# Kernel tuning notes

Hardware: AMD Instinct MI355X
Metric: run time of the kernel (lower is better)

## Reference

```python
import jax, jax.numpy as jnp
import numpy as np

B, H, W, D, C = 1, 32, 32, 32, 256
WS = (8, 8, 8)
SS = (4, 4, 4)
NH = 8
HD = C // NH
N = WS[0] * WS[1] * WS[2]
NW = (H // WS[0]) * (W // WS[1]) * (D // WS[2])


def _rel_pos_index():
    coords = np.stack(np.meshgrid(np.arange(WS[0]), np.arange(WS[1]), np.arange(WS[2]), indexing='ij'))
    cf = coords.reshape(3, -1)
    rc = (cf[:, :, None] - cf[:, None, :]).transpose(1, 2, 0).astype(np.int64)
    rc[:, :, 0] += WS[0] - 1
    rc[:, :, 1] += WS[1] - 1
    rc[:, :, 2] += WS[2] - 1
    rc[:, :, 0] *= (2 * WS[2] - 1) * (2 * WS[1] - 1)
    rc[:, :, 1] *= (2 * WS[2] - 1)
    return rc.sum(-1).reshape(-1)  # [N*N]


def _attn_mask():
    m = np.zeros((H, W, D), np.float32)
    cnt = 0

    def sl(ws, ss):
        return ((0, -ws), (-ws, -ss), (-ss, None))

    for hs in sl(WS[0], SS[0]):
        for ws_ in sl(WS[1], SS[1]):
            for ds in sl(WS[2], SS[2]):
                m[hs[0]:hs[1], ws_[0]:ws_[1], ds[0]:ds[1]] = cnt
                cnt += 1
    m = m.reshape(H // WS[0], WS[0], W // WS[1], WS[1], D // WS[2], WS[2])
    m = m.transpose(0, 2, 4, 1, 3, 5).reshape(NW, N)
    diff = m[:, None, :] - m[:, :, None]  # [NW, N, N]
    return np.where(diff != 0, -100.0, 0.0).astype(np.float32)


REL_IDX = jnp.asarray(_rel_pos_index())
ATTN_MASK = jnp.asarray(_attn_mask())  # [NW, N, N]


def setup_inputs() -> dict:
    key = jax.random.key(0)
    ks = jax.random.split(key, 4)
    return {
        'x': jax.random.normal(ks[0], (B, H, W, D, C), jnp.float32),
        'qkv_weight': jax.random.normal(ks[1], (3 * C, C), jnp.float32) * 0.02,
        'qkv_bias': jnp.zeros((3 * C,), jnp.float32),
        'proj_weight': jax.random.normal(ks[2], (C, C), jnp.float32) * 0.02,
        'proj_bias': jnp.zeros((C,), jnp.float32),
        'rpb_table': jax.random.normal(ks[3], ((2 * WS[0] - 1) * (2 * WS[1] - 1) * (2 * WS[2] - 1), NH), jnp.float32) * 0.02,
    }


def reference(x, qkv_weight, qkv_bias, proj_weight, proj_bias, rpb_table):
    # cyclic shift
    xs = jnp.roll(x, (-SS[0], -SS[1], -SS[2]), axis=(1, 2, 3))
    # window partition -> [B*NW, N, C]
    xw = xs.reshape(B, H // WS[0], WS[0], W // WS[1], WS[1], D // WS[2], WS[2], C)
    xw = xw.transpose(0, 1, 3, 5, 2, 4, 6, 7).reshape(B * NW, N, C)
    # qkv projection
    qkv = xw @ qkv_weight.T + qkv_bias
    qkv = qkv.reshape(B * NW, N, 3, NH, HD).transpose(2, 0, 3, 1, 4)  # [3, B*NW, NH, N, HD]
    q, k, v = qkv[0] * (HD ** -0.5), qkv[1], qkv[2]
    # relative position bias [NH, N, N]
    bias = rpb_table[REL_IDX].reshape(N, N, NH).transpose(2, 0, 1)
    attn = jnp.einsum('whnd,whmd->whnm', q, k) + bias[None]
    # shift mask per window
    attn = attn.reshape(B, NW, NH, N, N) + ATTN_MASK[None, :, None]
    attn = jax.nn.softmax(attn.reshape(B * NW, NH, N, N), axis=-1)
    out = jnp.einsum('whnm,whmd->whnd', attn, v)
    out = out.transpose(0, 2, 1, 3).reshape(B * NW, N, C)
    out = out @ proj_weight.T + proj_bias
    # un-window -> [B, H, W, D, C]
    out = out.reshape(B, H // WS[0], W // WS[1], D // WS[2], WS[0], WS[1], WS[2], C)
    out = out.transpose(0, 1, 4, 2, 5, 3, 6, 7).reshape(B, H, W, D, C)
    # reverse cyclic shift
    return jnp.roll(out, (SS[0], SS[1], SS[2]), axis=(1, 2, 3))
```

## Files before the change

### kernel.cpp

```cpp
#include <hip/hip_runtime.h>

typedef __attribute__((ext_vector_type(8))) short short8;
typedef __attribute__((ext_vector_type(4))) short s4v;
typedef __attribute__((ext_vector_type(2))) uint uint2v;
typedef __attribute__((ext_vector_type(4))) float floatx4;

#define CCH   256
#define QSCALE 0.17677669529663687f
#define LOG2E  1.4426950408889634f

__device__ __forceinline__ unsigned short f2bf(float f) {
    unsigned u = __float_as_uint(f);
    u = u + 0x7fffu + ((u >> 16) & 1u);
    return (unsigned short)(u >> 16);
}

__device__ __forceinline__ uint pk2bf(float a, float b) {
    uint ua = __float_as_uint(a) + 0x8000u;
    uint ub = __float_as_uint(b) + 0x8000u;
    return __builtin_amdgcn_perm(ub, ua, 0x07060302u);
}

__device__ __forceinline__ void gl_lds16(const void* g, void* l) {
    __builtin_amdgcn_global_load_lds((const __attribute__((address_space(1))) void*)g,
                                     (__attribute__((address_space(3))) void*)l, 16, 0, 0);
}

__device__ __forceinline__ int spatial_off(int token) {
    int w = token >> 9, n = token & 511;
    int wh = w >> 4, ww = (w >> 2) & 3, wd = w & 3;
    int h1 = n >> 6, w1 = (n >> 3) & 7, d1 = n & 7;
    int gh = (wh * 8 + h1 + 4) & 31;
    int gw = (ww * 8 + w1 + 4) & 31;
    int gd = (wd * 8 + d1 + 4) & 31;
    return ((gh * 32 + gw) * 32 + gd) * CCH;
}

__global__ __launch_bounds__(256) void xconv(const float* __restrict__ x,
                                             ushort* __restrict__ Xw) {
    int tid = blockIdx.x * 256 + threadIdx.x;
    int token = tid >> 5, c8 = (tid & 31) * 8;
    const float* src = x + spatial_off(token) + c8;
    float4 a = *(const float4*)src;
    float4 b = *(const float4*)(src + 4);
    uint2v lo, hi;
    lo[0] = pk2bf(a.x, a.y);
    lo[1] = pk2bf(a.z, a.w);
    hi[0] = pk2bf(b.x, b.y);
    hi[1] = pk2bf(b.z, b.w);
    uint2v* dst = (uint2v*)(Xw + (size_t)token * 256 + c8);
    dst[0] = lo;
    dst[1] = hi;
}

__global__ __launch_bounds__(256) void wconv(const float* __restrict__ Wq,
                                             const float* __restrict__ Wp,
                                             ushort* __restrict__ Wqb,
                                             ushort* __restrict__ Wpb) {
    int tid = blockIdx.x * 256 + threadIdx.x;
    if (tid < 196608) {
        float s = (tid < 65536) ? (QSCALE * LOG2E) : 1.0f;
        Wqb[tid] = f2bf(Wq[tid] * s);
    } else {
        int i = tid - 196608;
        Wpb[i] = f2bf(Wp[i]);
    }
}

__global__ __launch_bounds__(256) void pair_prep(const float* __restrict__ rpb,
                                                 uint* __restrict__ Up) {
    int tid = blockIdx.x * 256 + threadIdx.x;
    if (tid >= 27000) return;
    int head = tid / 3375, idx = tid - head * 3375;
    uint lo = f2bf(rpb[idx * 8 + head] * LOG2E);
    uint hi = f2bf(rpb[(idx > 0 ? idx - 1 : 0) * 8 + head] * LOG2E);
    Up[tid] = lo | (hi << 16);
}

__global__ __launch_bounds__(256) void gemm_qkv(
    const ushort* __restrict__ A,
    const ushort* __restrict__ Bw,
    const float* __restrict__ bq,
    ushort* __restrict__ Q, ushort* __restrict__ K, ushort* __restrict__ Vf) {
    __shared__ short As[128 * 64];
    __shared__ short Bs[128 * 64];
    const int t = threadIdx.x;
    const int wv = t >> 6, lane = t & 63, quad = lane >> 4, col = lane & 15;
    const int m0 = blockIdx.y * 128, n0 = blockIdx.x * 128;
    const int wm = (wv & 1) * 64, wn = (wv >> 1) * 64;

    floatx4 zf = {0.f, 0.f, 0.f, 0.f};
    floatx4 acc[4][4];
#pragma unroll
    for (int i = 0; i < 4; ++i)
#pragma unroll
        for (int j = 0; j < 4; ++j) acc[i][j] = zf;

    for (int kk = 0; kk < 256; kk += 64) {
        __syncthreads();
#pragma unroll
        for (int i = 0; i < 4; ++i) {
            int s = i * 256 + t;
            int row = s >> 3, qs = s & 7;
            int qg = qs ^ (row & 7);
            gl_lds16(A + (size_t)(m0 + row) * 256 + kk + qg * 8,
                     As + (i * 256 + wv * 64) * 8);
        }
#pragma unroll
        for (int i = 0; i < 4; ++i) {
            int s = i * 256 + t;
            int row = s >> 3, qs = s & 7;
            int qg = qs ^ (row & 7);
            gl_lds16(Bw + (size_t)(n0 + row) * 256 + kk + qg * 8,
                     Bs + (i * 256 + wv * 64) * 8);
        }
        __syncthreads();
#pragma unroll
        for (int h = 0; h < 2; ++h) {
            short8 af[4], bf[4];
#pragma unroll
            for (int mi = 0; mi < 4; ++mi) {
                int row = wm + mi * 16 + col;
                af[mi] = *(const short8*)(As + (row * 8 + ((h * 4 + quad) ^ (row & 7))) * 8);
            }
#pragma unroll
            for (int ni = 0; ni < 4; ++ni) {
                int row = wn + ni * 16 + col;
                bf[ni] = *(const short8*)(Bs + (row * 8 + ((h * 4 + quad) ^ (row & 7))) * 8);
            }
#pragma unroll
            for (int mi = 0; mi < 4; ++mi)
#pragma unroll
                for (int ni = 0; ni < 4; ++ni)
                    acc[mi][ni] = __builtin_amdgcn_mfma_f32_16x16x32_bf16(af[mi], bf[ni], acc[mi][ni], 0, 0, 0);
        }
    }

#pragma unroll
    for (int ni = 0; ni < 4; ++ni) {
        int j = n0 + wn + ni * 16 + col;
        int three = j >> 8, head = (j >> 5) & 7, hd = j & 31;
        float bias = bq[j] * ((j < 256) ? (QSCALE * LOG2E) : 1.0f);
        if (three == 2) {
            int h = hd >> 4, colv = hd & 15;
#pragma unroll
            for (int mi = 0; mi < 4; ++mi) {
                int mb = m0 + wm + mi * 16 + quad * 4;
                int w = mb >> 9, n = mb & 511;
                size_t off = ((size_t)((w * 8 + head) * 64 + (n >> 4) * 2 + h) << 8)
                           + ((((n >> 2) & 3) * 16 + colv) << 2);
                uint2v pv;
                pv[0] = pk2bf(acc[mi][ni][0] + bias, acc[mi][ni][1] + bias);
                pv[1] = pk2bf(acc[mi][ni][2] + bias, acc[mi][ni][3] + bias);
                *(uint2v*)(Vf + off) = pv;
            }
        } else if (three == 1) {
#pragma unroll
            for (int mi = 0; mi < 4; ++mi) {
#pragma unroll
                for (int r = 0; r < 4; ++r) {
                    int m = m0 + wm + mi * 16 + quad * 4 + r;
                    int w = m >> 9, n = m & 511;
                    size_t off = ((size_t)(w * 8 + head) << 14) + ((size_t)(n >> 4) << 9)
                               + (((hd >> 3) * 16 + (n & 15)) << 3) + (hd & 7);
                    K[off] = f2bf(acc[mi][ni][r] + bias);
                }
            }
        } else {
#pragma unroll
            for (int mi = 0; mi < 4; ++mi) {
#pragma unroll
                for (int r = 0; r < 4; ++r) {
                    int m = m0 + wm + mi * 16 + quad * 4 + r;
                    int w = m >> 9, n = m & 511;
                    Q[((size_t)(w * 8 + head) * 512 + n) * 32 + hd] = f2bf(acc[mi][ni][r] + bias);
                }
            }
        }
    }
}

__global__ __launch_bounds__(256) void gemm_proj(
    const ushort* __restrict__ A,
    const ushort* __restrict__ Bw,
    const float* __restrict__ bp,
    float* __restrict__ out) {
    __shared__ short As[128 * 64];
    __shared__ short Bs[128 * 64];
    const int t = threadIdx.x;
    const int wv = t >> 6, lane = t & 63, quad = lane >> 4, col = lane & 15;
    const int m0 = blockIdx.y * 128, n0 = blockIdx.x * 128;
    const int wm = (wv & 1) * 64, wn = (wv >> 1) * 64;

    floatx4 zf = {0.f, 0.f, 0.f, 0.f};
    floatx4 acc[4][4];
#pragma unroll
    for (int i = 0; i < 4; ++i)
#pragma unroll
        for (int j = 0; j < 4; ++j) acc[i][j] = zf;

    for (int kk = 0; kk < 256; kk += 64) {
        __syncthreads();
#pragma unroll
        for (int i = 0; i < 4; ++i) {
            int s = i * 256 + t;
            int row = s >> 3, qs = s & 7;
            int qg = qs ^ (row & 7);
            gl_lds16(A + (size_t)(m0 + row) * 256 + kk + qg * 8,
                     As + (i * 256 + wv * 64) * 8);
        }
#pragma unroll
        for (int i = 0; i < 4; ++i) {
            int s = i * 256 + t;
            int row = s >> 3, qs = s & 7;
            int qg = qs ^ (row & 7);
            gl_lds16(Bw + (size_t)(n0 + row) * 256 + kk + qg * 8,
                     Bs + (i * 256 + wv * 64) * 8);
        }
        __syncthreads();
#pragma unroll
        for (int h = 0; h < 2; ++h) {
            short8 af[4], bf[4];
#pragma unroll
            for (int mi = 0; mi < 4; ++mi) {
                int row = wm + mi * 16 + col;
                af[mi] = *(const short8*)(As + (row * 8 + ((h * 4 + quad) ^ (row & 7))) * 8);
            }
#pragma unroll
            for (int ni = 0; ni < 4; ++ni) {
                int row = wn + ni * 16 + col;
                bf[ni] = *(const short8*)(Bs + (row * 8 + ((h * 4 + quad) ^ (row & 7))) * 8);
            }
#pragma unroll
            for (int mi = 0; mi < 4; ++mi)
#pragma unroll
                for (int ni = 0; ni < 4; ++ni)
                    acc[mi][ni] = __builtin_amdgcn_mfma_f32_16x16x32_bf16(af[mi], bf[ni], acc[mi][ni], 0, 0, 0);
        }
    }

#pragma unroll
    for (int ni = 0; ni < 4; ++ni) {
        int j = n0 + wn + ni * 16 + col;
        float bias = bp[j];
#pragma unroll
        for (int mi = 0; mi < 4; ++mi) {
#pragma unroll
            for (int r = 0; r < 4; ++r) {
                int m = m0 + wm + mi * 16 + quad * 4 + r;
                out[spatial_off(m) + j] = acc[mi][ni][r] + bias;
            }
        }
    }
}

__global__ __launch_bounds__(512, 2) void attn_kernel(
    const ushort* __restrict__ Q, const ushort* __restrict__ K,
    const ushort* __restrict__ Vf, const uint* __restrict__ Up,
    ushort* __restrict__ Y) {
    __shared__ short Kl[512 * 32];
    __shared__ short Vs[64 * 256];
    __shared__ uint  Ul[3375];

    const int t = threadIdx.x;
    const int bid = blockIdx.x;
    const int w = bid >> 3, head = bid & 7;
    const int wh = w >> 4, ww = (w >> 2) & 3, wd = w & 3;
    const int wv = t >> 6, lane = t & 63, quad = lane >> 4, col = lane & 15;

    const ushort* Kg = K + (size_t)(w * 8 + head) * 512 * 32;
    const ushort* Vg = Vf + (size_t)(w * 8 + head) * 512 * 32;
    const ushort* Qg = Q + (size_t)(w * 8 + head) * 512 * 32;

#pragma unroll
    for (int i = 0; i < 4; ++i) {
        gl_lds16(Kg + (size_t)(i * 512 + t) * 8, Kl + (i * 512 + wv * 64) * 8);
        gl_lds16(Vg + (size_t)(i * 512 + t) * 8, Vs + (i * 512 + wv * 64) * 8);
    }
    const uint* Uph = Up + head * 3375;
    for (int i = t; i < 3375; i += 512) Ul[i] = Uph[i];
    __syncthreads();

    const bool boundary = (wh == 3) | (ww == 3) | (wd == 3);
    floatx4 zf = {0.f, 0.f, 0.f, 0.f};

    for (int qs = 0; qs < 4; ++qs) {
        const int qt = wv * 4 + qs;
        const short8 qf = *(const short8*)(Qg + (size_t)(qt * 16 + col) * 32 + quad * 8);

        const int qrow = qt * 16 + col;
        const int qh = qrow >> 6, qw = (qrow >> 3) & 7, qd = qrow & 7;
        const int Base0 = ((qh + 7) * 15 + (qw + 7 - (quad >> 1))) * 15
                        + (qd - ((quad & 1) << 2) + 7);
        const int cq = ((wh == 3) ? (1 + ((qrow >> 8) & 1)) * 16 : 0)
                     + ((ww == 3) ? (1 + ((qrow >> 5) & 1)) * 4 : 0)
                     + ((wd == 3) ? (1 + ((qrow >> 2) & 1)) : 0);

        float rs = 0.f;
        floatx4 o0 = zf, o1 = zf;

        for (int c = 0; c < 2; ++c) {
            const short* KlC = Kl + c * 8192;
            const short* VsC = Vs + c * 8192;
            const int BaseC = Base0 - c * 900;
            const int ckh = (wh == 3) ? ((1 + c) * 16) : 0;

            floatx4 acc[16];
#pragma unroll
            for (int tt = 0; tt < 16; ++tt) {
                const int Kt2 = ((tt >> 2) * 15 + (tt & 3) * 2) * 15;
                uint p0 = Ul[BaseC - Kt2];
                uint p1 = Ul[BaseC - Kt2 - 2];
                floatx4 cf;
                cf[0] = __uint_as_float(p0 << 16);
                cf[1] = __uint_as_float(p0 & 0xffff0000u);
                cf[2] = __uint_as_float(p1 << 16);
                cf[3] = __uint_as_float(p1 & 0xffff0000u);
                if (boundary) {
                    int ck = ckh
                           + ((ww == 3) ? (1 + ((tt >> 1) & 1)) * 4 : 0)
                           + ((wd == 3) ? (1 + (quad & 1)) : 0);
                    float madd = (cq == ck) ? 0.f : -144.269504f;
                    cf[0] += madd; cf[1] += madd; cf[2] += madd; cf[3] += madd;
                }
                short8 kf = *(const short8*)(KlC + tt * 512 + lane * 8);
                acc[tt] = __builtin_amdgcn_mfma_f32_16x16x32_bf16(kf, qf, cf, 0, 0, 0);
            }

#pragma unroll
            for (int tt = 0; tt < 16; ++tt) {
                float e0 = __builtin_amdgcn_exp2f(acc[tt][0]);
                float e1 = __builtin_amdgcn_exp2f(acc[tt][1]);
                float e2 = __builtin_amdgcn_exp2f(acc[tt][2]);
                float e3 = __builtin_amdgcn_exp2f(acc[tt][3]);
                rs += (e0 + e1) + (e2 + e3);
                uint2v pp;
                pp[0] = pk2bf(e0, e1);
                pp[1] = pk2bf(e2, e3);
                s4v pf = __builtin_bit_cast(s4v, pp);
                s4v v0 = *(const s4v*)(VsC + ((tt * 2 + 0) << 8) + lane * 4);
                s4v v1 = *(const s4v*)(VsC + ((tt * 2 + 1) << 8) + lane * 4);
                o0 = __builtin_amdgcn_mfma_f32_16x16x16bf16_1k(v0, pf, o0, 0, 0, 0);
                o1 = __builtin_amdgcn_mfma_f32_16x16x16bf16_1k(v1, pf, o1, 0, 0, 0);
            }
        }

        rs += __shfl_xor(rs, 16);
        rs += __shfl_xor(rs, 32);
        const float inv = __builtin_amdgcn_rcpf(rs);

        int token = w * 512 + qt * 16 + col;
        ushort* Yb = Y + (size_t)token * 256 + head * 32 + quad * 4;
        uint2v y0, y1;
        y0[0] = pk2bf(o0[0] * inv, o0[1] * inv);
        y0[1] = pk2bf(o0[2] * inv, o0[3] * inv);
        y1[0] = pk2bf(o1[0] * inv, o1[1] * inv);
        y1[1] = pk2bf(o1[2] * inv, o1[3] * inv);
        *(uint2v*)(Yb) = y0;
        *(uint2v*)(Yb + 16) = y1;
    }
}

extern "C" void kernel_launch(void* const* d_in, const int* in_sizes, int n_in,
                              void* d_out, int out_size, void* d_ws, size_t ws_size,
                              hipStream_t stream) {
    const float* x      = (const float*)d_in[0];
    const float* qkv_w  = (const float*)d_in[1];
    const float* qkv_b  = (const float*)d_in[2];
    const float* proj_w = (const float*)d_in[3];
    const float* proj_b = (const float*)d_in[4];
    const float* rpb    = (const float*)d_in[5];
    float* out = (float*)d_out;

    ushort* Xw  = (ushort*)d_ws;
    ushort* Q   = Xw + 8388608;
    ushort* K   = Q + 8388608;
    ushort* Vf  = K + 8388608;
    ushort* Y   = Vf + 8388608;
    uint*   Up  = (uint*)(Y + 8388608);
    ushort* Wqb = (ushort*)(Up + 27008);
    ushort* Wpb = Wqb + 196608;

    xconv<<<dim3(4096), dim3(256), 0, stream>>>(x, Xw);
    wconv<<<dim3(1024), dim3(256), 0, stream>>>(qkv_w, proj_w, Wqb, Wpb);
    pair_prep<<<dim3(106), dim3(256), 0, stream>>>(rpb, Up);
    gemm_qkv<<<dim3(6, 256), dim3(256), 0, stream>>>(Xw, Wqb, qkv_b, Q, K, Vf);
    attn_kernel<<<dim3(512), dim3(512), 0, stream>>>(Q, K, Vf, Up, Y);
    gemm_proj<<<dim3(2, 256), dim3(256), 0, stream>>>(Y, Wpb, proj_b, out);
}
```

Baseline: 177.1 us.

## Merge prep kernels and stage Q/K epilogue through LDS for vectorized stores

Combines the three small conversion kernels (x, weights, rel-pos bias) into a single launch dispatched by block index range, which removes two kernel launches. In the QKV GEMM, the Q and K outputs are now written to a padded shared-memory tile first and then stored to global memory as 16-byte vectors in their target layouts, replacing scattered 2-byte stores. The V path keeps its direct packed stores. The staging adds two barriers and more LDS (the shared buffer is enlarged) per block in the Q/K columns.

```diff
diff --git a/kernel.cpp b/kernel.cpp
--- a/kernel.cpp
+++ b/kernel.cpp
@@ -3,6 +3,7 @@
 typedef __attribute__((ext_vector_type(8))) short short8;
 typedef __attribute__((ext_vector_type(4))) short s4v;
 typedef __attribute__((ext_vector_type(2))) uint uint2v;
+typedef __attribute__((ext_vector_type(4))) uint uint4v;
 typedef __attribute__((ext_vector_type(4))) float floatx4;
 
 #define CCH   256
@@ -36,45 +37,46 @@
     return ((gh * 32 + gw) * 32 + gd) * CCH;
 }
 
-__global__ __launch_bounds__(256) void xconv(const float* __restrict__ x,
-                                             ushort* __restrict__ Xw) {
-    int tid = blockIdx.x * 256 + threadIdx.x;
-    int token = tid >> 5, c8 = (tid & 31) * 8;
-    const float* src = x + spatial_off(token) + c8;
-    float4 a = *(const float4*)src;
-    float4 b = *(const float4*)(src + 4);
-    uint2v lo, hi;
-    lo[0] = pk2bf(a.x, a.y);
-    lo[1] = pk2bf(a.z, a.w);
-    hi[0] = pk2bf(b.x, b.y);
-    hi[1] = pk2bf(b.z, b.w);
-    uint2v* dst = (uint2v*)(Xw + (size_t)token * 256 + c8);
-    dst[0] = lo;
-    dst[1] = hi;
-}
-
-__global__ __launch_bounds__(256) void wconv(const float* __restrict__ Wq,
-                                             const float* __restrict__ Wp,
-                                             ushort* __restrict__ Wqb,
-                                             ushort* __restrict__ Wpb) {
-    int tid = blockIdx.x * 256 + threadIdx.x;
-    if (tid < 196608) {
-        float s = (tid < 65536) ? (QSCALE * LOG2E) : 1.0f;
-        Wqb[tid] = f2bf(Wq[tid] * s);
+__global__ __launch_bounds__(256) void prep(const float* __restrict__ x,
+                                            const float* __restrict__ Wq,
+                                            const float* __restrict__ Wp,
+                                            const float* __restrict__ rpb,
+                                            ushort* __restrict__ Xw,
+                                            ushort* __restrict__ Wqb,
+                                            ushort* __restrict__ Wpb,
+                                            uint* __restrict__ Up) {
+    int b = blockIdx.x;
+    if (b < 4096) {
+        int tid = b * 256 + threadIdx.x;
+        int token = tid >> 5, c8 = (tid & 31) * 8;
+        const float* src = x + spatial_off(token) + c8;
+        float4 a = *(const float4*)src;
+        float4 bb = *(const float4*)(src + 4);
+        uint2v lo, hi;
+        lo[0] = pk2bf(a.x, a.y);
+        lo[1] = pk2bf(a.z, a.w);
+        hi[0] = pk2bf(bb.x, bb.y);
+        hi[1] = pk2bf(bb.z, bb.w);
+        uint2v* dst = (uint2v*)(Xw + (size_t)token * 256 + c8);
+        dst[0] = lo;
+        dst[1] = hi;
+    } else if (b < 5120) {
+        int tid = (b - 4096) * 256 + threadIdx.x;
+        if (tid < 196608) {
+            float s = (tid < 65536) ? (QSCALE * LOG2E) : 1.0f;
+            Wqb[tid] = f2bf(Wq[tid] * s);
+        } else {
+            int i = tid - 196608;
+            Wpb[i] = f2bf(Wp[i]);
+        }
     } else {
-        int i = tid - 196608;
-        Wpb[i] = f2bf(Wp[i]);
-    }
-}
-
-__global__ __launch_bounds__(256) void pair_prep(const float* __restrict__ rpb,
-                                                 uint* __restrict__ Up) {
-    int tid = blockIdx.x * 256 + threadIdx.x;
-    if (tid >= 27000) return;
-    int head = tid / 3375, idx = tid - head * 3375;
-    uint lo = f2bf(rpb[idx * 8 + head] * LOG2E);
-    uint hi = f2bf(rpb[(idx > 0 ? idx - 1 : 0) * 8 + head] * LOG2E);
-    Up[tid] = lo | (hi << 16);
+        int tid = (b - 5120) * 256 + threadIdx.x;
+        if (tid >= 27000) return;
+        int head = tid / 3375, idx = tid - head * 3375;
+        uint lo = f2bf(rpb[idx * 8 + head] * LOG2E);
+        uint hi = f2bf(rpb[(idx > 0 ? idx - 1 : 0) * 8 + head] * LOG2E);
+        Up[tid] = lo | (hi << 16);
+    }
 }
 
 __global__ __launch_bounds__(256) void gemm_qkv(
@@ -82,8 +84,9 @@
     const ushort* __restrict__ Bw,
     const float* __restrict__ bq,
     ushort* __restrict__ Q, ushort* __restrict__ K, ushort* __restrict__ Vf) {
-    __shared__ short As[128 * 64];
-    __shared__ short Bs[128 * 64];
+    __shared__ short Sh[17408];
+    short* As = Sh;
+    short* Bs = Sh + 8192;
     const int t = threadIdx.x;
     const int wv = t >> 6, lane = t & 63, quad = lane >> 4, col = lane & 15;
     const int m0 = blockIdx.y * 128, n0 = blockIdx.x * 128;
@@ -136,12 +139,13 @@
         }
     }
 
-#pragma unroll
-    for (int ni = 0; ni < 4; ++ni) {
-        int j = n0 + wn + ni * 16 + col;
-        int three = j >> 8, head = (j >> 5) & 7, hd = j & 31;
-        float bias = bq[j] * ((j < 256) ? (QSCALE * LOG2E) : 1.0f);
-        if (three == 2) {
+    const int bx = blockIdx.x;
+    if (bx >= 4) {
+#pragma unroll
+        for (int ni = 0; ni < 4; ++ni) {
+            int j = n0 + wn + ni * 16 + col;
+            int head = (j >> 5) & 7, hd = j & 31;
+            float bias = bq[j];
             int h = hd >> 4, colv = hd & 15;
 #pragma unroll
             for (int mi = 0; mi < 4; ++mi) {
@@ -154,28 +158,42 @@
                 pv[1] = pk2bf(acc[mi][ni][2] + bias, acc[mi][ni][3] + bias);
                 *(uint2v*)(Vf + off) = pv;
             }
-        } else if (three == 1) {
+        }
+    } else {
+        __syncthreads();
+#pragma unroll
+        for (int ni = 0; ni < 4; ++ni) {
+            int j = n0 + wn + ni * 16 + col;
+            int jloc = wn + ni * 16 + col;
+            float bias = bq[j] * ((j < 256) ? (QSCALE * LOG2E) : 1.0f);
 #pragma unroll
             for (int mi = 0; mi < 4; ++mi) {
-#pragma unroll
-                for (int r = 0; r < 4; ++r) {
-                    int m = m0 + wm + mi * 16 + quad * 4 + r;
-                    int w = m >> 9, n = m & 511;
-                    size_t off = ((size_t)(w * 8 + head) << 14) + ((size_t)(n >> 4) << 9)
-                               + (((hd >> 3) * 16 + (n & 15)) << 3) + (hd & 7);
-                    K[off] = f2bf(acc[mi][ni][r] + bias);
-                }
-            }
-        } else {
-#pragma unroll
-            for (int mi = 0; mi < 4; ++mi) {
-#pragma unroll
-                for (int r = 0; r < 4; ++r) {
-                    int m = m0 + wm + mi * 16 + quad * 4 + r;
-                    int w = m >> 9, n = m & 511;
-                    Q[((size_t)(w * 8 + head) * 512 + n) * 32 + hd] = f2bf(acc[mi][ni][r] + bias);
-                }
-            }
+                int rowb = wm + mi * 16 + quad * 4;
+#pragma unroll
+                for (int r = 0; r < 4; ++r)
+                    Sh[(rowb + r) * 136 + jloc] = (short)f2bf(acc[mi][ni][r] + bias);
+            }
+        }
+        __syncthreads();
+        ushort* dst = (bx < 2) ? Q : K;
+#pragma unroll
+        for (int k8 = 0; k8 < 8; ++k8) {
+            int chunk = k8 * 256 + t;
+            int row = chunk >> 4;
+            int jl = (chunk & 15) * 8;
+            int j = n0 + jl;
+            int m = m0 + row;
+            int w = m >> 9, n = m & 511;
+            int head = (j >> 5) & 7, hd = j & 31;
+            uint4v vv = *(const uint4v*)(Sh + row * 136 + jl);
+            size_t off;
+            if (bx < 2) {
+                off = ((size_t)(w * 8 + head) * 512 + n) * 32 + hd;
+            } else {
+                off = ((size_t)(w * 8 + head) << 14) + ((size_t)(n >> 4) << 9)
+                    + (((hd >> 3) * 16 + (n & 15)) << 3);
+            }
+            *(uint4v*)(dst + off) = vv;
         }
     }
 }
@@ -381,9 +399,7 @@
     ushort* Wqb = (ushort*)(Up + 27008);
     ushort* Wpb = Wqb + 196608;
 
-    xconv<<<dim3(4096), dim3(256), 0, stream>>>(x, Xw);
-    wconv<<<dim3(1024), dim3(256), 0, stream>>>(qkv_w, proj_w, Wqb, Wpb);
-    pair_prep<<<dim3(106), dim3(256), 0, stream>>>(rpb, Up);
+    prep<<<dim3(5226), dim3(256), 0, stream>>>(x, qkv_w, proj_w, rpb, Xw, Wqb, Wpb, Up);
     gemm_qkv<<<dim3(6, 256), dim3(256), 0, stream>>>(Xw, Wqb, qkv_b, Q, K, Vf);
     attn_kernel<<<dim3(512), dim3(512), 0, stream>>>(Q, K, Vf, Up, Y);
     gemm_proj<<<dim3(2, 256), dim3(256), 0, stream>>>(Y, Wpb, proj_b, out);
```

Result: faster. 172.0 us (-2.9%).
